# Kernel optimization log

Hardware: AMD Instinct MI355X
Metric: run time of the kernel (lower is better)

Reference implementation:

```python
import jax, jax.numpy as jnp
import numpy as np


def _row_distance(a, b):
    # pairwise cosine similarity between rows of a [N,D] and b [K,D] -> [N,K]
    an = a / (jnp.linalg.norm(a, axis=1, keepdims=True) + 1e-12)
    bn = b / (jnp.linalg.norm(b, axis=1, keepdims=True) + 1e-12)
    return an @ bn.T


def _nearest_context(feature, context):
    sim = _row_distance(feature, context)          # [B, K]
    # distances = -sim; argmin(distances) == argmax(sim)
    min_ind = jnp.argmax(sim, axis=1)              # [B]
    onehot = jax.nn.one_hot(min_ind, context.shape[0], dtype=feature.dtype)  # [B, K]
    rslt = onehot @ jax.lax.stop_gradient(context)  # [B, E] codebook gather
    return rslt, onehot


@jax.custom_vjp
def _vq(feature, context):
    return _nearest_context(feature, context)[0]


def _vq_fwd(feature, context):
    value, ind = _nearest_context(feature, context)
    return value, ind


def _vq_bwd(ind, d_value):
    # straight-through to feature; scatter grads into codebook rows
    return (d_value, ind.T @ d_value)


_vq.defvjp(_vq_fwd, _vq_bwd)


def setup_inputs() -> dict:
    key = jax.random.key(0)
    ks = jax.random.split(key, 6)
    B, FEAT, MID, EMB, K = 8192, 4096, 512, 256, 512
    return {
        "x": jax.random.normal(ks[0], (B, FEAT), dtype=jnp.float32),
        "enc_w1": jax.random.normal(ks[1], (FEAT, MID), dtype=jnp.float32) * 0.02,
        "enc_b1": jnp.zeros((MID,), dtype=jnp.float32),
        "enc_w2": jax.random.normal(ks[2], (MID, EMB), dtype=jnp.float32) * 0.02,
        "enc_b2": jnp.zeros((EMB,), dtype=jnp.float32),
        "emb": jax.random.normal(ks[3], (K, EMB), dtype=jnp.float32) * 0.01,
        "dec_w1": jax.random.normal(ks[4], (EMB, MID), dtype=jnp.float32) * 0.02,
        "dec_b1": jnp.zeros((MID,), dtype=jnp.float32),
        "dec_w2": jax.random.normal(ks[5], (MID, FEAT), dtype=jnp.float32) * 0.02,
        "dec_b2": jnp.zeros((FEAT,), dtype=jnp.float32),
    }


def reference(x, enc_w1, enc_b1, enc_w2, enc_b2, emb, dec_w1, dec_b1, dec_w2, dec_b2):
    # encoder (stand-in for MultiContextEncoder with out_size=(middle_dim, emb_dim))
    h = jax.nn.relu(x @ enc_w1 + enc_b1)           # [B, MID]
    encoded = h @ enc_w2 + enc_b2                  # [B, EMB]
    # vector quantization with straight-through gradient
    vq_feat = _vq(encoded, emb)                    # [B, EMB]
    _, context_ind = _nearest_context(encoded, emb)  # [B, K] one-hot
    # decoder: Dense(middle_dim, relu) -> Dense(feat_dim, relu)
    d = jax.nn.relu(vq_feat @ dec_w1 + dec_b1)     # [B, MID]
    decoded = jax.nn.relu(d @ dec_w2 + dec_b2)     # [B, FEAT]
    return (encoded, vq_feat, context_ind, decoded, emb)
```

## Files before the change

### kernel.cpp

```cpp
#include <hip/hip_runtime.h>

#define BATCH 8192
#define FEAT  4096
#define MID   512
#define EMB   256
#define KCODE 512

typedef _Float16 half8 __attribute__((ext_vector_type(8)));
typedef _Float16 half4v __attribute__((ext_vector_type(4)));
typedef float floatx4 __attribute__((ext_vector_type(4)));

#define SC_X    512.0f
#define SC_W    4096.0f
#define SC_H    512.0f
#define SC_ENC  4096.0f
#define SC_CODE 4096.0f
#define SC_EMB  4096.0f
#define SC_TM   512.0f
#define DS_G1   (1.0f / (SC_X   * SC_W))
#define DS_G2   (1.0f / (SC_H   * SC_W))
#define DS_D1   (1.0f / (SC_EMB * SC_W))
#define DS_D2   (1.0f / (SC_TM  * SC_W))

#define GLD16(gp, lp)                                                          \
    __builtin_amdgcn_global_load_lds(                                          \
        (const __attribute__((address_space(1))) void*)(gp),                   \
        (__attribute__((address_space(3))) void*)(lp), 16, 0, 0)

template<int NT, int AF32>
__global__ __launch_bounds__(256)
void gemm_sk(const float* __restrict__ Af32,
             const _Float16* __restrict__ Ahg, const _Float16* __restrict__ Alg,
             const _Float16* __restrict__ BTh, const _Float16* __restrict__ BTl,
             float aScale,
             float* __restrict__ partOut,
             const float* __restrict__ bias, float descale, int relu,
             float* __restrict__ outF, _Float16* __restrict__ outHi,
             _Float16* __restrict__ outLo, float outScale,
             int M, int N, int K, int lgK, int lgN, int swz)
{
    __shared__ _Float16 AhS[2][128 * 32];
    __shared__ _Float16 BhS[2][128 * 32];
    __shared__ _Float16 AlS[NT == 3 ? 2 : 1][NT == 3 ? 128 * 32 : 8];
    __shared__ _Float16 BlS[NT == 3 ? 2 : 1][NT == 3 ? 128 * 32 : 8];

    const int tid  = threadIdx.x;
    const int lane = tid & 63;
    const int wave = tid >> 6;
    const int wm = wave >> 1, wn = wave & 1;
    const int l15  = lane & 15;
    const int quad = lane >> 4;
    const int q8   = quad * 8;

    int bm, bn, ks;
    if (swz) {
        int b = blockIdx.x;
        int mlo = b & 7;
        ks = (b >> 3) & ((1 << lgK) - 1);
        bn = (b >> (3 + lgK)) & ((1 << lgN) - 1);
        bm = ((b >> (3 + lgK + lgN)) << 3) | mlo;
    } else { bm = blockIdx.y; bn = blockIdx.x; ks = 0; }
    const int row0 = bm * 128, col0 = bn * 128;
    const int Kslice = K >> lgK;
    const int k0 = ks * Kslice;

    const int sr4 = tid >> 2;
    const int sc4 = (tid & 3) * 8;
    const size_t aB0 = (size_t)(row0 + sr4) * K + sc4;
    const size_t aB1 = (size_t)(row0 + 64 + sr4) * K + sc4;
    const size_t bB0 = (size_t)(col0 + sr4) * K + sc4;
    const size_t bB1 = (size_t)(col0 + 64 + sr4) * K + sc4;
    const int l0 = tid * 8, l1 = 2048 + tid * 8;

    const int sr2 = tid >> 1;
    const int sk2 = (tid & 1) * 16;
    const size_t aOff2 = (size_t)(row0 + sr2) * K + sk2;
    const int lA = sr2 * 32 + sk2;

    floatx4 acc[4][4] = {};

    auto cvtA = [&](int s, float4 f0, float4 f1, float4 f2, float4 f3) {
        float fv[16] = {f0.x,f0.y,f0.z,f0.w, f1.x,f1.y,f1.z,f1.w,
                        f2.x,f2.y,f2.z,f2.w, f3.x,f3.y,f3.z,f3.w};
        half8 hv0, hv1, lv0, lv1;
        #pragma unroll
        for (int e = 0; e < 8; ++e) {
            float v = fv[e] * aScale;
            _Float16 h = (_Float16)v;
            hv0[e] = h; lv0[e] = (_Float16)(v - (float)h);
        }
        #pragma unroll
        for (int e = 0; e < 8; ++e) {
            float v = fv[8 + e] * aScale;
            _Float16 h = (_Float16)v;
            hv1[e] = h; lv1[e] = (_Float16)(v - (float)h);
        }
        *(half8*)&AhS[s][lA] = hv0; *(half8*)&AhS[s][lA + 8] = hv1;
        if (NT == 3) {
            *(half8*)&AlS[s][lA] = lv0; *(half8*)&AlS[s][lA + 8] = lv1;
        }
    };

    const int Ksteps = Kslice >> 5;

    {
        if (AF32) {
            const float* p = Af32 + aOff2 + k0;
            float4 f0 = *(const float4*)(p);
            float4 f1 = *(const float4*)(p + 4);
            float4 f2 = *(const float4*)(p + 8);
            float4 f3 = *(const float4*)(p + 12);
            cvtA(0, f0, f1, f2, f3);
        } else {
            GLD16(Ahg + aB0 + k0, &AhS[0][l0]);
            GLD16(Ahg + aB1 + k0, &AhS[0][l1]);
            if (NT == 3) {
                GLD16(Alg + aB0 + k0, &AlS[0][l0]);
                GLD16(Alg + aB1 + k0, &AlS[0][l1]);
            }
        }
        GLD16(BTh + bB0 + k0, &BhS[0][l0]);
        GLD16(BTh + bB1 + k0, &BhS[0][l1]);
        if (NT == 3) {
            GLD16(BTl + bB0 + k0, &BlS[0][l0]);
            GLD16(BTl + bB1 + k0, &BlS[0][l1]);
        }
        if (AF32) {
            asm volatile("s_waitcnt lgkmcnt(0)" ::: "memory");
        }
    }

    for (int it = 0; it < Ksteps; ++it) {
        const int cur = it & 1, nxt = cur ^ 1;
        const bool pf = (it + 1) < Ksteps;
        float4 f0, f1, f2, f3;
        if (pf) {
            const int kk = k0 + (it + 1) * 32;
            if (AF32) {
                const float* p = Af32 + aOff2 + kk;
                f0 = *(const float4*)(p);
                f1 = *(const float4*)(p + 4);
                f2 = *(const float4*)(p + 8);
                f3 = *(const float4*)(p + 12);
            } else {
                GLD16(Ahg + aB0 + kk, &AhS[nxt][l0]);
                GLD16(Ahg + aB1 + kk, &AhS[nxt][l1]);
                if (NT == 3) {
                    GLD16(Alg + aB0 + kk, &AlS[nxt][l0]);
                    GLD16(Alg + aB1 + kk, &AlS[nxt][l1]);
                }
            }
            GLD16(BTh + bB0 + kk, &BhS[nxt][l0]);
            GLD16(BTh + bB1 + kk, &BhS[nxt][l1]);
            if (NT == 3) {
                GLD16(BTl + bB0 + kk, &BlS[nxt][l0]);
                GLD16(BTl + bB1 + kk, &BlS[nxt][l1]);
            }
            if constexpr (NT == 3)
                asm volatile("s_waitcnt vmcnt(8)" ::: "memory");
            else if constexpr (AF32)
                asm volatile("s_waitcnt vmcnt(6)" ::: "memory");
            else
                asm volatile("s_waitcnt vmcnt(4)" ::: "memory");
        } else {
            asm volatile("s_waitcnt vmcnt(0)" ::: "memory");
        }
        __builtin_amdgcn_s_barrier();

        half8 ah[4], al4[4], bh[4], bl4[4];
        #pragma unroll
        for (int i = 0; i < 4; ++i) {
            int ra = (wm * 64 + i * 16 + l15) * 32 + q8;
            int rb = (wn * 64 + i * 16 + l15) * 32 + q8;
            ah[i] = *(const half8*)&AhS[cur][ra];
            bh[i] = *(const half8*)&BhS[cur][rb];
            if (NT == 3) {
                al4[i] = *(const half8*)&AlS[cur][ra];
                bl4[i] = *(const half8*)&BlS[cur][rb];
            }
        }
        #pragma unroll
        for (int i = 0; i < 4; ++i)
            #pragma unroll
            for (int j = 0; j < 4; ++j) {
                acc[i][j] = __builtin_amdgcn_mfma_f32_16x16x32_f16(ah[i], bh[j], acc[i][j], 0, 0, 0);
                if (NT == 3) {
                    acc[i][j] = __builtin_amdgcn_mfma_f32_16x16x32_f16(ah[i],  bl4[j], acc[i][j], 0, 0, 0);
                    acc[i][j] = __builtin_amdgcn_mfma_f32_16x16x32_f16(al4[i], bh[j],  acc[i][j], 0, 0, 0);
                }
            }
        if (AF32 && pf) {
            cvtA(nxt, f0, f1, f2, f3);
            asm volatile("s_waitcnt lgkmcnt(0)" ::: "memory");
        }
        __builtin_amdgcn_s_barrier();
    }

    if (partOut) {
        float* po = partOut + (size_t)ks * M * N;
        #pragma unroll
        for (int j = 0; j < 4; ++j) {
            int col = col0 + wn * 64 + j * 16 + l15;
            #pragma unroll
            for (int i = 0; i < 4; ++i)
                #pragma unroll
                for (int t = 0; t < 4; ++t) {
                    int r = row0 + wm * 64 + i * 16 + quad * 4 + t;
                    po[(size_t)r * N + col] = acc[i][j][t];
                }
        }
    } else {
        #pragma unroll
        for (int j = 0; j < 4; ++j) {
            int col = col0 + wn * 64 + j * 16 + l15;
            float bcol = bias ? bias[col] : 0.0f;
            #pragma unroll
            for (int i = 0; i < 4; ++i)
                #pragma unroll
                for (int t = 0; t < 4; ++t) {
                    int r = row0 + wm * 64 + i * 16 + quad * 4 + t;
                    float v = acc[i][j][t] * descale + bcol;
                    if (relu) v = fmaxf(v, 0.0f);
                    size_t o = (size_t)r * N + col;
                    if (outF) outF[o] = v;
                    if (outHi) {
                        float sv = v * outScale;
                        _Float16 h = (_Float16)sv;
                        outHi[o] = h;
                        outLo[o] = (_Float16)(sv - (float)h);
                    }
                }
        }
    }
}

__global__ __launch_bounds__(256)
void reduce_sk(const float* __restrict__ part, int nSlice, int MN, int N,
               const float* __restrict__ bias, float descale, int relu,
               float* __restrict__ outF, _Float16* __restrict__ outHi,
               _Float16* __restrict__ outLo, float outScale)
{
    int i = blockIdx.x * 256 + threadIdx.x;
    if (i * 4 >= MN) return;
    float4 s = ((const float4*)part)[i];
    for (int sl = 1; sl < nSlice; ++sl) {
        float4 p = ((const float4*)(part + (size_t)sl * MN))[i];
        s.x += p.x; s.y += p.y; s.z += p.z; s.w += p.w;
    }
    int col = (i * 4) % N;
    float v[4] = {s.x, s.y, s.z, s.w};
    #pragma unroll
    for (int e = 0; e < 4; ++e) {
        float t = v[e] * descale + (bias ? bias[col + e] : 0.0f);
        if (relu) t = fmaxf(t, 0.0f);
        v[e] = t;
    }
    if (outF) ((float4*)outF)[i] = *(float4*)v;
    if (outHi) {
        half4v hv, lv;
        #pragma unroll
        for (int e = 0; e < 4; ++e) {
            float sv = v[e] * outScale;
            _Float16 h = (_Float16)sv;
            hv[e] = h;
            lv[e] = (_Float16)(sv - (float)h);
        }
        ((half4v*)outHi)[i] = hv;
        ((half4v*)outLo)[i] = lv;
    }
}

__global__ __launch_bounds__(256)
void transpose_split(const float* __restrict__ src, _Float16* __restrict__ hi,
                     _Float16* __restrict__ lo, float scale, int R, int C)
{
    __shared__ float t[32][33];
    int tx = threadIdx.x & 31, ty = threadIdx.x >> 5;
    int r0 = blockIdx.y * 32, c0 = blockIdx.x * 32;
    #pragma unroll
    for (int p = 0; p < 4; ++p) {
        int r = ty + p * 8;
        t[r][tx] = src[(size_t)(r0 + r) * C + c0 + tx];
    }
    __syncthreads();
    #pragma unroll
    for (int p = 0; p < 4; ++p) {
        int oc = ty + p * 8;
        float v = t[tx][oc] * scale;
        _Float16 h = (_Float16)v;
        size_t o = (size_t)(c0 + oc) * R + r0 + tx;
        hi[o] = h;
        lo[o] = (_Float16)(v - (float)h);
    }
}

__global__ __launch_bounds__(256)
void norm_codes(const float* __restrict__ emb, _Float16* __restrict__ cnHi,
                _Float16* __restrict__ cnLo)
{
    int wave = threadIdx.x >> 6;
    int lane = threadIdx.x & 63;
    int c = blockIdx.x * 4 + wave;
    if (c >= KCODE) return;
    const float* er = emb + (size_t)c * EMB;
    float ss = 0.0f;
    #pragma unroll
    for (int k = lane; k < EMB; k += 64) { float v = er[k]; ss += v * v; }
    #pragma unroll
    for (int off = 32; off > 0; off >>= 1) ss += __shfl_down(ss, off, 64);
    ss = __shfl(ss, 0, 64);
    float inv = 1.0f / (sqrtf(ss) + 1e-12f);
    #pragma unroll
    for (int k = lane; k < EMB; k += 64) {
        float v = er[k] * inv * SC_CODE;
        _Float16 h = (_Float16)v;
        cnHi[(size_t)c * EMB + k] = h;
        cnLo[(size_t)c * EMB + k] = (_Float16)(v - (float)h);
    }
}

__global__ __launch_bounds__(256)
void argmax_vq3(const float* __restrict__ part, int MN,
                const float* __restrict__ emb,
                const float* __restrict__ Dcode,
                float* __restrict__ onehot, float* __restrict__ vqfeat,
                float* __restrict__ decoded)
{
    __shared__ int sBest;
    const int row = blockIdx.x;
    const int tid = threadIdx.x;

    if (tid < 64) {
        const float* p0 = part + (size_t)row * KCODE;
        const float* p1 = part + (size_t)MN + (size_t)row * KCODE;
        float bestV = -3.402823466e+38f;
        int   bestI = 0;
        #pragma unroll
        for (int c = tid; c < KCODE; c += 64) {
            float v = p0[c] + p1[c];
            if (v > bestV) { bestV = v; bestI = c; }
        }
        #pragma unroll
        for (int off = 32; off > 0; off >>= 1) {
            float ov = __shfl_down(bestV, off, 64);
            int   oi = __shfl_down(bestI, off, 64);
            if (ov > bestV || (ov == bestV && oi < bestI)) { bestV = ov; bestI = oi; }
        }
        if (tid == 0) sBest = bestI;
    }
    __syncthreads();
    const int bestI = sBest;

    float* oh = onehot + (size_t)row * KCODE;
    oh[tid]       = (tid       == bestI) ? 1.0f : 0.0f;
    oh[tid + 256] = (tid + 256 == bestI) ? 1.0f : 0.0f;

    vqfeat[(size_t)row * EMB + tid] = emb[(size_t)bestI * EMB + tid];

    const float4* sd = (const float4*)(Dcode + (size_t)bestI * FEAT);
    float4* dd = (float4*)(decoded + (size_t)row * FEAT);
    #pragma unroll
    for (int i = tid; i < FEAT / 4; i += 256) dd[i] = sd[i];
}

__global__ __launch_bounds__(256)
void copy_f4(const float* __restrict__ src, float* __restrict__ dst, int n4)
{
    int i = blockIdx.x * 256 + threadIdx.x;
    if (i < n4) ((float4*)dst)[i] = ((const float4*)src)[i];
}

extern "C" void kernel_launch(void* const* d_in, const int* in_sizes, int n_in,
                              void* d_out, int out_size, void* d_ws, size_t ws_size,
                              hipStream_t stream)
{
    const float* x      = (const float*)d_in[0];
    const float* enc_w1 = (const float*)d_in[1];
    const float* enc_b1 = (const float*)d_in[2];
    const float* enc_w2 = (const float*)d_in[3];
    const float* enc_b2 = (const float*)d_in[4];
    const float* emb    = (const float*)d_in[5];
    const float* dec_w1 = (const float*)d_in[6];
    const float* dec_b1 = (const float*)d_in[7];
    const float* dec_w2 = (const float*)d_in[8];
    const float* dec_b2 = (const float*)d_in[9];

    float* out = (float*)d_out;
    float* out_encoded = out;
    float* out_vqfeat  = out + (size_t)BATCH * EMB;
    float* out_onehot  = out + (size_t)2 * BATCH * EMB;
    float* out_decoded = out + (size_t)2 * BATCH * EMB + (size_t)BATCH * KCODE;
    float* out_emb     = out_decoded + (size_t)BATCH * FEAT;

    char* w = (char*)d_ws;
    _Float16* w1T_hi = (_Float16*)w;  w += (size_t)FEAT * MID * 2;
    _Float16* w1T_lo = (_Float16*)w;  w += (size_t)FEAT * MID * 2;
    _Float16* w2T_hi = (_Float16*)w;  w += (size_t)MID * EMB * 2;
    _Float16* w2T_lo = (_Float16*)w;  w += (size_t)MID * EMB * 2;
    _Float16* wd1T_hi= (_Float16*)w;  w += (size_t)MID * EMB * 2;
    _Float16* wd1T_lo= (_Float16*)w;  w += (size_t)MID * EMB * 2;
    _Float16* wd2T_hi= (_Float16*)w;  w += (size_t)FEAT * MID * 2;
    _Float16* wd2T_lo= (_Float16*)w;  w += (size_t)FEAT * MID * 2;
    _Float16* h_hi   = (_Float16*)w;  w += (size_t)BATCH * MID * 2;
    _Float16* h_lo   = (_Float16*)w;  w += (size_t)BATCH * MID * 2;
    _Float16* enc_hi = (_Float16*)w;  w += (size_t)BATCH * EMB * 2;
    _Float16* enc_lo = (_Float16*)w;  w += (size_t)BATCH * EMB * 2;
    _Float16* cn_hi  = (_Float16*)w;  w += (size_t)KCODE * EMB * 2;
    _Float16* cn_lo  = (_Float16*)w;  w += (size_t)KCODE * EMB * 2;
    _Float16* tm_hi  = (_Float16*)w;  w += (size_t)KCODE * MID * 2;
    _Float16* tm_lo  = (_Float16*)w;  w += (size_t)KCODE * MID * 2;
    float*    Dc     = (float*)w;     w += (size_t)KCODE * FEAT * 4;
    float*    scr    = (float*)w;     w += (size_t)4 * BATCH * MID * 4;

    transpose_split<<<dim3(MID / 32, FEAT / 32), dim3(256), 0, stream>>>(
        enc_w1, w1T_hi, w1T_lo, SC_W, FEAT, MID);
    transpose_split<<<dim3(EMB / 32, MID / 32), dim3(256), 0, stream>>>(
        enc_w2, w2T_hi, w2T_lo, SC_W, MID, EMB);
    transpose_split<<<dim3(MID / 32, EMB / 32), dim3(256), 0, stream>>>(
        dec_w1, wd1T_hi, wd1T_lo, SC_W, EMB, MID);
    transpose_split<<<dim3(FEAT / 32, MID / 32), dim3(256), 0, stream>>>(
        dec_w2, wd2T_hi, wd2T_lo, SC_W, MID, FEAT);
    norm_codes<<<dim3(KCODE / 4), dim3(256), 0, stream>>>(emb, cn_hi, cn_lo);
    copy_f4<<<dim3((KCODE * EMB / 4 + 255) / 256), dim3(256), 0, stream>>>(
        emb, out_emb, KCODE * EMB / 4);

    gemm_sk<1, 1><<<dim3(KCODE / 128, KCODE / 128), dim3(256), 0, stream>>>(
        emb, nullptr, nullptr, wd1T_hi, wd1T_lo, SC_EMB,
        nullptr, dec_b1, DS_D1, 1, nullptr, tm_hi, tm_lo, SC_TM,
        KCODE, MID, EMB, 0, 0, 0);
    gemm_sk<1, 0><<<dim3(FEAT / 128, KCODE / 128), dim3(256), 0, stream>>>(
        nullptr, tm_hi, tm_lo, wd2T_hi, wd2T_lo, 0.0f,
        nullptr, dec_b2, DS_D2, 1, Dc, nullptr, nullptr, 0.0f,
        KCODE, FEAT, MID, 0, 0, 0);

    gemm_sk<3, 1><<<dim3(512), dim3(256), 0, stream>>>(
        x, nullptr, nullptr, w1T_hi, w1T_lo, SC_X,
        scr, nullptr, 0.0f, 0, nullptr, nullptr, nullptr, 0.0f,
        BATCH, MID, FEAT, 1, 2, 1);
    reduce_sk<<<dim3(BATCH * MID / 4 / 256), dim3(256), 0, stream>>>(
        scr, 2, BATCH * MID, MID, enc_b1, DS_G1, 1,
        nullptr, h_hi, h_lo, SC_H);

    gemm_sk<3, 0><<<dim3(512), dim3(256), 0, stream>>>(
        nullptr, h_hi, h_lo, w2T_hi, w2T_lo, 0.0f,
        scr, nullptr, 0.0f, 0, nullptr, nullptr, nullptr, 0.0f,
        BATCH, EMB, MID, 2, 1, 1);
    reduce_sk<<<dim3(BATCH * EMB / 4 / 256), dim3(256), 0, stream>>>(
        scr, 4, BATCH * EMB, EMB, enc_b2, DS_G2, 0,
        out_encoded, enc_hi, enc_lo, SC_ENC);

    gemm_sk<3, 0><<<dim3(512), dim3(256), 0, stream>>>(
        nullptr, enc_hi, enc_lo, cn_hi, cn_lo, 0.0f,
        scr, nullptr, 0.0f, 0, nullptr, nullptr, nullptr, 0.0f,
        BATCH, KCODE, EMB, 1, 2, 1);
    argmax_vq3<<<dim3(BATCH), dim3(256), 0, stream>>>(
        scr, BATCH * KCODE, emb, Dc, out_onehot, out_vqfeat, out_decoded);
}
```

Measured before the change: 487.0 us.

## Fuse split-K reduction of first encoder GEMM into second GEMM's A load; merge prep kernels

The second encoder GEMM now reads the two fp32 split-K partials of the first GEMM directly. It sums them, applies descale, bias and ReLU, and splits the result into hi/lo fp16 in its A-tile loader. This removes the separate reduce_sk pass and the h_hi/h_lo round trip through memory. The four weight transposes, the codebook normalization and the emb copy are also merged into one launch to cut launch count. In exchange, each K step of the fused GEMM issues more global loads and does more conversion arithmetic, and the reduction work is repeated for each N-tile block.

```diff
diff --git a/kernel.cpp b/kernel.cpp
--- a/kernel.cpp
+++ b/kernel.cpp
@@ -27,12 +27,13 @@
         (const __attribute__((address_space(1))) void*)(gp),                   \
         (__attribute__((address_space(3))) void*)(lp), 16, 0, 0)
 
-template<int NT, int AF32>
+template<int NT, int ASRC>
 __global__ __launch_bounds__(256)
 void gemm_sk(const float* __restrict__ Af32,
              const _Float16* __restrict__ Ahg, const _Float16* __restrict__ Alg,
              const _Float16* __restrict__ BTh, const _Float16* __restrict__ BTl,
              float aScale,
+             const float* __restrict__ redBias, float redDS, int redMN,
              float* __restrict__ partOut,
              const float* __restrict__ bias, float descale, int relu,
              float* __restrict__ outF, _Float16* __restrict__ outHi,
@@ -79,7 +80,7 @@
 
     floatx4 acc[4][4] = {};
 
-    auto cvtA = [&](int s, float4 f0, float4 f1, float4 f2, float4 f3) {
+    auto cvtA1 = [&](int s, float4 f0, float4 f1, float4 f2, float4 f3) {
         float fv[16] = {f0.x,f0.y,f0.z,f0.w, f1.x,f1.y,f1.z,f1.w,
                         f2.x,f2.y,f2.z,f2.w, f3.x,f3.y,f3.z,f3.w};
         half8 hv0, hv1, lv0, lv1;
@@ -101,31 +102,75 @@
         }
     };
 
+    auto cvtA2 = [&](int s,
+                     float4 A0, float4 A1, float4 A2, float4 A3,
+                     float4 C0, float4 C1, float4 C2, float4 C3,
+                     float4 B0, float4 B1, float4 B2, float4 B3) {
+        float sv[16] = {A0.x+C0.x, A0.y+C0.y, A0.z+C0.z, A0.w+C0.w,
+                        A1.x+C1.x, A1.y+C1.y, A1.z+C1.z, A1.w+C1.w,
+                        A2.x+C2.x, A2.y+C2.y, A2.z+C2.z, A2.w+C2.w,
+                        A3.x+C3.x, A3.y+C3.y, A3.z+C3.z, A3.w+C3.w};
+        float bv[16] = {B0.x,B0.y,B0.z,B0.w, B1.x,B1.y,B1.z,B1.w,
+                        B2.x,B2.y,B2.z,B2.w, B3.x,B3.y,B3.z,B3.w};
+        half8 hv0, hv1, lv0, lv1;
+        #pragma unroll
+        for (int e = 0; e < 8; ++e) {
+            float t = sv[e] * redDS + bv[e];
+            t = fmaxf(t, 0.0f);
+            float v = t * aScale;
+            _Float16 h = (_Float16)v;
+            hv0[e] = h; lv0[e] = (_Float16)(v - (float)h);
+        }
+        #pragma unroll
+        for (int e = 0; e < 8; ++e) {
+            float t = sv[8 + e] * redDS + bv[8 + e];
+            t = fmaxf(t, 0.0f);
+            float v = t * aScale;
+            _Float16 h = (_Float16)v;
+            hv1[e] = h; lv1[e] = (_Float16)(v - (float)h);
+        }
+        *(half8*)&AhS[s][lA] = hv0; *(half8*)&AhS[s][lA + 8] = hv1;
+        *(half8*)&AlS[s][lA] = lv0; *(half8*)&AlS[s][lA + 8] = lv1;
+    };
+
     const int Ksteps = Kslice >> 5;
 
+    constexpr int PFW = (ASRC == 2) ? 16 : (NT == 3 ? 8 : (ASRC == 1 ? 6 : 4));
+
     {
-        if (AF32) {
+        if constexpr (ASRC == 0) {
+            GLD16(Ahg + aB0 + k0, &AhS[0][l0]);
+            GLD16(Ahg + aB1 + k0, &AhS[0][l1]);
+            if (NT == 3) {
+                GLD16(Alg + aB0 + k0, &AlS[0][l0]);
+                GLD16(Alg + aB1 + k0, &AlS[0][l1]);
+            }
+        }
+        GLD16(BTh + bB0 + k0, &BhS[0][l0]);
+        GLD16(BTh + bB1 + k0, &BhS[0][l1]);
+        if (NT == 3) {
+            GLD16(BTl + bB0 + k0, &BlS[0][l0]);
+            GLD16(BTl + bB1 + k0, &BlS[0][l1]);
+        }
+        if constexpr (ASRC == 1) {
             const float* p = Af32 + aOff2 + k0;
             float4 f0 = *(const float4*)(p);
             float4 f1 = *(const float4*)(p + 4);
             float4 f2 = *(const float4*)(p + 8);
             float4 f3 = *(const float4*)(p + 12);
-            cvtA(0, f0, f1, f2, f3);
-        } else {
-            GLD16(Ahg + aB0 + k0, &AhS[0][l0]);
-            GLD16(Ahg + aB1 + k0, &AhS[0][l1]);
-            if (NT == 3) {
-                GLD16(Alg + aB0 + k0, &AlS[0][l0]);
-                GLD16(Alg + aB1 + k0, &AlS[0][l1]);
-            }
-        }
-        GLD16(BTh + bB0 + k0, &BhS[0][l0]);
-        GLD16(BTh + bB1 + k0, &BhS[0][l1]);
-        if (NT == 3) {
-            GLD16(BTl + bB0 + k0, &BlS[0][l0]);
-            GLD16(BTl + bB1 + k0, &BlS[0][l1]);
-        }
-        if (AF32) {
+            cvtA1(0, f0, f1, f2, f3);
+            asm volatile("s_waitcnt lgkmcnt(0)" ::: "memory");
+        } else if constexpr (ASRC == 2) {
+            const float* p0 = Af32 + aOff2 + k0;
+            const float* p1 = p0 + redMN;
+            const float* pb = redBias + k0 + sk2;
+            float4 A0 = ((const float4*)p0)[0], A1 = ((const float4*)p0)[1];
+            float4 A2 = ((const float4*)p0)[2], A3 = ((const float4*)p0)[3];
+            float4 C0 = ((const float4*)p1)[0], C1 = ((const float4*)p1)[1];
+            float4 C2 = ((const float4*)p1)[2], C3 = ((const float4*)p1)[3];
+            float4 B0 = ((const float4*)pb)[0], B1 = ((const float4*)pb)[1];
+            float4 B2 = ((const float4*)pb)[2], B3 = ((const float4*)pb)[3];
+            cvtA2(0, A0,A1,A2,A3, C0,C1,C2,C3, B0,B1,B2,B3);
             asm volatile("s_waitcnt lgkmcnt(0)" ::: "memory");
         }
     }
@@ -134,21 +179,32 @@
         const int cur = it & 1, nxt = cur ^ 1;
         const bool pf = (it + 1) < Ksteps;
         float4 f0, f1, f2, f3;
+        float4 A0, A1, A2, A3, C0, C1, C2, C3, B0, B1, B2, B3;
         if (pf) {
             const int kk = k0 + (it + 1) * 32;
-            if (AF32) {
+            if constexpr (ASRC == 0) {
+                GLD16(Ahg + aB0 + kk, &AhS[nxt][l0]);
+                GLD16(Ahg + aB1 + kk, &AhS[nxt][l1]);
+                if (NT == 3) {
+                    GLD16(Alg + aB0 + kk, &AlS[nxt][l0]);
+                    GLD16(Alg + aB1 + kk, &AlS[nxt][l1]);
+                }
+            } else if constexpr (ASRC == 1) {
                 const float* p = Af32 + aOff2 + kk;
                 f0 = *(const float4*)(p);
                 f1 = *(const float4*)(p + 4);
                 f2 = *(const float4*)(p + 8);
                 f3 = *(const float4*)(p + 12);
             } else {
-                GLD16(Ahg + aB0 + kk, &AhS[nxt][l0]);
-                GLD16(Ahg + aB1 + kk, &AhS[nxt][l1]);
-                if (NT == 3) {
-                    GLD16(Alg + aB0 + kk, &AlS[nxt][l0]);
-                    GLD16(Alg + aB1 + kk, &AlS[nxt][l1]);
-                }
+                const float* p0 = Af32 + aOff2 + kk;
+                const float* p1 = p0 + redMN;
+                const float* pb = redBias + kk + sk2;
+                A0 = ((const float4*)p0)[0]; A1 = ((const float4*)p0)[1];
+                A2 = ((const float4*)p0)[2]; A3 = ((const float4*)p0)[3];
+                C0 = ((const float4*)p1)[0]; C1 = ((const float4*)p1)[1];
+                C2 = ((const float4*)p1)[2]; C3 = ((const float4*)p1)[3];
+                B0 = ((const float4*)pb)[0]; B1 = ((const float4*)pb)[1];
+                B2 = ((const float4*)pb)[2]; B3 = ((const float4*)pb)[3];
             }
             GLD16(BTh + bB0 + kk, &BhS[nxt][l0]);
             GLD16(BTh + bB1 + kk, &BhS[nxt][l1]);
@@ -156,12 +212,7 @@
                 GLD16(BTl + bB0 + kk, &BlS[nxt][l0]);
                 GLD16(BTl + bB1 + kk, &BlS[nxt][l1]);
             }
-            if constexpr (NT == 3)
-                asm volatile("s_waitcnt vmcnt(8)" ::: "memory");
-            else if constexpr (AF32)
-                asm volatile("s_waitcnt vmcnt(6)" ::: "memory");
-            else
-                asm volatile("s_waitcnt vmcnt(4)" ::: "memory");
+            asm volatile("s_waitcnt vmcnt(%0)" :: "i"(PFW) : "memory");
         } else {
             asm volatile("s_waitcnt vmcnt(0)" ::: "memory");
         }
@@ -189,9 +240,16 @@
                     acc[i][j] = __builtin_amdgcn_mfma_f32_16x16x32_f16(al4[i], bh[j],  acc[i][j], 0, 0, 0);
                 }
             }
-        if (AF32 && pf) {
-            cvtA(nxt, f0, f1, f2, f3);
-            asm volatile("s_waitcnt lgkmcnt(0)" ::: "memory");
+        if constexpr (ASRC == 1) {
+            if (pf) {
+                cvtA1(nxt, f0, f1, f2, f3);
+                asm volatile("s_waitcnt lgkmcnt(0)" ::: "memory");
+            }
+        } else if constexpr (ASRC == 2) {
+            if (pf) {
+                cvtA2(nxt, A0,A1,A2,A3, C0,C1,C2,C3, B0,B1,B2,B3);
+                asm volatile("s_waitcnt lgkmcnt(0)" ::: "memory");
+            }
         }
         __builtin_amdgcn_s_barrier();
     }
@@ -270,13 +328,13 @@
     }
 }
 
-__global__ __launch_bounds__(256)
-void transpose_split(const float* __restrict__ src, _Float16* __restrict__ hi,
-                     _Float16* __restrict__ lo, float scale, int R, int C)
+__device__ __forceinline__ void transpose_body(
+    float (*t)[33],
+    const float* __restrict__ src, _Float16* __restrict__ hi,
+    _Float16* __restrict__ lo, float scale, int R, int C, int bx, int by)
 {
-    __shared__ float t[32][33];
     int tx = threadIdx.x & 31, ty = threadIdx.x >> 5;
-    int r0 = blockIdx.y * 32, c0 = blockIdx.x * 32;
+    int r0 = by * 32, c0 = bx * 32;
     #pragma unroll
     for (int p = 0; p < 4; ++p) {
         int r = ty + p * 8;
@@ -295,27 +353,50 @@
 }
 
 __global__ __launch_bounds__(256)
-void norm_codes(const float* __restrict__ emb, _Float16* __restrict__ cnHi,
-                _Float16* __restrict__ cnLo)
+void prep_fused(const float* __restrict__ enc_w1, const float* __restrict__ enc_w2,
+                const float* __restrict__ dec_w1, const float* __restrict__ dec_w2,
+                const float* __restrict__ emb,
+                _Float16* __restrict__ w1T_hi, _Float16* __restrict__ w1T_lo,
+                _Float16* __restrict__ w2T_hi, _Float16* __restrict__ w2T_lo,
+                _Float16* __restrict__ wd1T_hi, _Float16* __restrict__ wd1T_lo,
+                _Float16* __restrict__ wd2T_hi, _Float16* __restrict__ wd2T_lo,
+                _Float16* __restrict__ cnHi, _Float16* __restrict__ cnLo,
+                float* __restrict__ out_emb)
 {
-    int wave = threadIdx.x >> 6;
-    int lane = threadIdx.x & 63;
-    int c = blockIdx.x * 4 + wave;
-    if (c >= KCODE) return;
-    const float* er = emb + (size_t)c * EMB;
-    float ss = 0.0f;
-    #pragma unroll
-    for (int k = lane; k < EMB; k += 64) { float v = er[k]; ss += v * v; }
-    #pragma unroll
-    for (int off = 32; off > 0; off >>= 1) ss += __shfl_down(ss, off, 64);
-    ss = __shfl(ss, 0, 64);
-    float inv = 1.0f / (sqrtf(ss) + 1e-12f);
-    #pragma unroll
-    for (int k = lane; k < EMB; k += 64) {
-        float v = er[k] * inv * SC_CODE;
-        _Float16 h = (_Float16)v;
-        cnHi[(size_t)c * EMB + k] = h;
-        cnLo[(size_t)c * EMB + k] = (_Float16)(v - (float)h);
+    __shared__ float t[32][33];
+    const int b = blockIdx.x;
+    if (b < 2048) {
+        transpose_body(t, enc_w1, w1T_hi, w1T_lo, SC_W, FEAT, MID, b & 15, b >> 4);
+    } else if (b < 2176) {
+        int bb = b - 2048;
+        transpose_body(t, enc_w2, w2T_hi, w2T_lo, SC_W, MID, EMB, bb & 7, bb >> 3);
+    } else if (b < 2304) {
+        int bb = b - 2176;
+        transpose_body(t, dec_w1, wd1T_hi, wd1T_lo, SC_W, EMB, MID, bb & 15, bb >> 4);
+    } else if (b < 4352) {
+        int bb = b - 2304;
+        transpose_body(t, dec_w2, wd2T_hi, wd2T_lo, SC_W, MID, FEAT, bb & 127, bb >> 7);
+    } else if (b < 4480) {
+        int wv = threadIdx.x >> 6, lane = threadIdx.x & 63;
+        int c = (b - 4352) * 4 + wv;
+        const float* er = emb + (size_t)c * EMB;
+        float ss = 0.0f;
+        #pragma unroll
+        for (int k = lane; k < EMB; k += 64) { float v = er[k]; ss += v * v; }
+        #pragma unroll
+        for (int off = 32; off > 0; off >>= 1) ss += __shfl_down(ss, off, 64);
+        ss = __shfl(ss, 0, 64);
+        float inv = 1.0f / (sqrtf(ss) + 1e-12f);
+        #pragma unroll
+        for (int k = lane; k < EMB; k += 64) {
+            float v = er[k] * inv * SC_CODE;
+            _Float16 h = (_Float16)v;
+            cnHi[(size_t)c * EMB + k] = h;
+            cnLo[(size_t)c * EMB + k] = (_Float16)(v - (float)h);
+        }
+    } else {
+        int i = (b - 4480) * 256 + threadIdx.x;
+        ((float4*)out_emb)[i] = ((const float4*)emb)[i];
     }
 }
 
@@ -361,13 +442,6 @@
     float4* dd = (float4*)(decoded + (size_t)row * FEAT);
     #pragma unroll
     for (int i = tid; i < FEAT / 4; i += 256) dd[i] = sd[i];
-}
-
-__global__ __launch_bounds__(256)
-void copy_f4(const float* __restrict__ src, float* __restrict__ dst, int n4)
-{
-    int i = blockIdx.x * 256 + threadIdx.x;
-    if (i < n4) ((float4*)dst)[i] = ((const float4*)src)[i];
 }
 
 extern "C" void kernel_launch(void* const* d_in, const int* in_sizes, int n_in,
@@ -401,8 +475,6 @@
     _Float16* wd1T_lo= (_Float16*)w;  w += (size_t)MID * EMB * 2;
     _Float16* wd2T_hi= (_Float16*)w;  w += (size_t)FEAT * MID * 2;
     _Float16* wd2T_lo= (_Float16*)w;  w += (size_t)FEAT * MID * 2;
-    _Float16* h_hi   = (_Float16*)w;  w += (size_t)BATCH * MID * 2;
-    _Float16* h_lo   = (_Float16*)w;  w += (size_t)BATCH * MID * 2;
     _Float16* enc_hi = (_Float16*)w;  w += (size_t)BATCH * EMB * 2;
     _Float16* enc_lo = (_Float16*)w;  w += (size_t)BATCH * EMB * 2;
     _Float16* cn_hi  = (_Float16*)w;  w += (size_t)KCODE * EMB * 2;
@@ -411,46 +483,42 @@
     _Float16* tm_lo  = (_Float16*)w;  w += (size_t)KCODE * MID * 2;
     float*    Dc     = (float*)w;     w += (size_t)KCODE * FEAT * 4;
     float*    scr    = (float*)w;     w += (size_t)4 * BATCH * MID * 4;
-
-    transpose_split<<<dim3(MID / 32, FEAT / 32), dim3(256), 0, stream>>>(
-        enc_w1, w1T_hi, w1T_lo, SC_W, FEAT, MID);
-    transpose_split<<<dim3(EMB / 32, MID / 32), dim3(256), 0, stream>>>(
-        enc_w2, w2T_hi, w2T_lo, SC_W, MID, EMB);
-    transpose_split<<<dim3(MID / 32, EMB / 32), dim3(256), 0, stream>>>(
-        dec_w1, wd1T_hi, wd1T_lo, SC_W, EMB, MID);
-    transpose_split<<<dim3(FEAT / 32, MID / 32), dim3(256), 0, stream>>>(
-        dec_w2, wd2T_hi, wd2T_lo, SC_W, MID, FEAT);
-    norm_codes<<<dim3(KCODE / 4), dim3(256), 0, stream>>>(emb, cn_hi, cn_lo);
-    copy_f4<<<dim3((KCODE * EMB / 4 + 255) / 256), dim3(256), 0, stream>>>(
-        emb, out_emb, KCODE * EMB / 4);
+    float*    scr2   = scr + (size_t)2 * BATCH * MID;
+
+    prep_fused<<<dim3(4608), dim3(256), 0, stream>>>(
+        enc_w1, enc_w2, dec_w1, dec_w2, emb,
+        w1T_hi, w1T_lo, w2T_hi, w2T_lo, wd1T_hi, wd1T_lo, wd2T_hi, wd2T_lo,
+        cn_hi, cn_lo, out_emb);
 
     gemm_sk<1, 1><<<dim3(KCODE / 128, KCODE / 128), dim3(256), 0, stream>>>(
         emb, nullptr, nullptr, wd1T_hi, wd1T_lo, SC_EMB,
+        nullptr, 0.0f, 0,
         nullptr, dec_b1, DS_D1, 1, nullptr, tm_hi, tm_lo, SC_TM,
         KCODE, MID, EMB, 0, 0, 0);
     gemm_sk<1, 0><<<dim3(FEAT / 128, KCODE / 128), dim3(256), 0, stream>>>(
         nullptr, tm_hi, tm_lo, wd2T_hi, wd2T_lo, 0.0f,
+        nullptr, 0.0f, 0,
         nullptr, dec_b2, DS_D2, 1, Dc, nullptr, nullptr, 0.0f,
         KCODE, FEAT, MID, 0, 0, 0);
 
     gemm_sk<3, 1><<<dim3(512), dim3(256), 0, stream>>>(
         x, nullptr, nullptr, w1T_hi, w1T_lo, SC_X,
+        nullptr, 0.0f, 0,
         scr, nullptr, 0.0f, 0, nullptr, nullptr, nullptr, 0.0f,
         BATCH, MID, FEAT, 1, 2, 1);
-    reduce_sk<<<dim3(BATCH * MID / 4 / 256), dim3(256), 0, stream>>>(
-        scr, 2, BATCH * MID, MID, enc_b1, DS_G1, 1,
-        nullptr, h_hi, h_lo, SC_H);
-
-    gemm_sk<3, 0><<<dim3(512), dim3(256), 0, stream>>>(
-        nullptr, h_hi, h_lo, w2T_hi, w2T_lo, 0.0f,
-        scr, nullptr, 0.0f, 0, nullptr, nullptr, nullptr, 0.0f,
+
+    gemm_sk<3, 2><<<dim3(512), dim3(256), 0, stream>>>(
+        scr, nullptr, nullptr, w2T_hi, w2T_lo, SC_H,
+        enc_b1, DS_G1, BATCH * MID,
+        scr2, nullptr, 0.0f, 0, nullptr, nullptr, nullptr, 0.0f,
         BATCH, EMB, MID, 2, 1, 1);
     reduce_sk<<<dim3(BATCH * EMB / 4 / 256), dim3(256), 0, stream>>>(
-        scr, 4, BATCH * EMB, EMB, enc_b2, DS_G2, 0,
+        scr2, 4, BATCH * EMB, EMB, enc_b2, DS_G2, 0,
         out_encoded, enc_hi, enc_lo, SC_ENC);
 
     gemm_sk<3, 0><<<dim3(512), dim3(256), 0, stream>>>(
         nullptr, enc_hi, enc_lo, cn_hi, cn_lo, 0.0f,
+        nullptr, 0.0f, 0,
         scr, nullptr, 0.0f, 0, nullptr, nullptr, nullptr, 0.0f,
         BATCH, KCODE, EMB, 1, 2, 1);
     argmax_vq3<<<dim3(BATCH), dim3(256), 0, stream>>>(
```

Result: faster. 465.4 us (-4.4%).
